# Optimization experiments

Hardware: AMD Instinct MI355X
Metric: run time of the kernel (lower is better)

The kernel has to match this reference:

```python
import jax, jax.numpy as jnp
import numpy as np

B, T, C, H, M = 2, 2048, 1024, 16, 64
EPS = 1e-5


def _ln(x, g, b):
    mu = jnp.mean(x, axis=-1, keepdims=True)
    var = jnp.mean(jnp.square(x - mu), axis=-1, keepdims=True)
    return (x - mu) * jax.lax.rsqrt(var + EPS) * g + b


def setup_inputs() -> dict:
    key = jax.random.key(0)
    ks = jax.random.split(key, 16)
    s = lambda fan_in: 1.0 / np.sqrt(fan_in)
    return {
        'x': jax.random.normal(ks[0], (B, T, C), jnp.float32),
        'ln1_g': jnp.ones((C,), jnp.float32),
        'ln1_b': jnp.zeros((C,), jnp.float32),
        'attn_w': jax.random.normal(ks[1], (C, 3 * C), jnp.float32) * s(C),
        'attn_b': jnp.zeros((3 * C,), jnp.float32),
        'proj_w': jax.random.normal(ks[2], (C, C), jnp.float32) * s(C),
        'proj_b': jnp.zeros((C,), jnp.float32),
        'a1_dw': jax.random.normal(ks[3], (C, M), jnp.float32) * s(C),
        'a1_db': jnp.zeros((M,), jnp.float32),
        'a1_uw': jax.random.normal(ks[4], (M, C), jnp.float32) * s(M),
        'a1_ub': jnp.zeros((C,), jnp.float32),
        'ln2_g': jnp.ones((C,), jnp.float32),
        'ln2_b': jnp.zeros((C,), jnp.float32),
        'fc_w': jax.random.normal(ks[5], (C, 4 * C), jnp.float32) * s(C),
        'fc_b': jnp.zeros((4 * C,), jnp.float32),
        'mlp_pw': jax.random.normal(ks[6], (4 * C, C), jnp.float32) * s(4 * C),
        'mlp_pb': jnp.zeros((C,), jnp.float32),
        'a2_dw': jax.random.normal(ks[7], (C, M), jnp.float32) * s(C),
        'a2_db': jnp.zeros((M,), jnp.float32),
        'a2_uw': jax.random.normal(ks[8], (M, C), jnp.float32) * s(M),
        'a2_ub': jnp.zeros((C,), jnp.float32),
    }


def _attn(x, attn_w, attn_b, proj_w, proj_b):
    b, t, c = x.shape
    hd = c // H
    qkv = x @ attn_w + attn_b                      # [B,T,3C]
    q, k, v = jnp.split(qkv, 3, axis=-1)
    q = q.reshape(b, t, H, hd).transpose(0, 2, 1, 3)  # [B,H,T,hd]
    k = k.reshape(b, t, H, hd).transpose(0, 2, 1, 3)
    v = v.reshape(b, t, H, hd).transpose(0, 2, 1, 3)
    att = jnp.einsum('bhqd,bhkd->bhqk', q, k) * (1.0 / np.sqrt(hd))
    mask = jnp.tril(jnp.ones((t, t), bool))
    att = jnp.where(mask, att, -jnp.inf)
    att = jax.nn.softmax(att, axis=-1)
    y = jnp.einsum('bhqk,bhkd->bhqd', att, v)      # [B,H,T,hd]
    y = y.transpose(0, 2, 1, 3).reshape(b, t, c)
    return y @ proj_w + proj_b


def _adapter(x, dw, db, uw, ub):
    return jax.nn.relu(x @ dw + db) @ uw + ub


def reference(x, ln1_g, ln1_b, attn_w, attn_b, proj_w, proj_b,
              a1_dw, a1_db, a1_uw, a1_ub, ln2_g, ln2_b,
              fc_w, fc_b, mlp_pw, mlp_pb, a2_dw, a2_db, a2_uw, a2_ub):
    x = x + _attn(_ln(x, ln1_g, ln1_b), attn_w, attn_b, proj_w, proj_b)
    x = x + _adapter(x, a1_dw, a1_db, a1_uw, a1_ub)
    h = _ln(x, ln2_g, ln2_b)
    h = jax.nn.gelu(h @ fc_w + fc_b, approximate=True) @ mlp_pw + mlp_pb
    x = x + h
    x = x + _adapter(x, a2_dw, a2_db, a2_uw, a2_ub)
    return x
```

## Files before the change

### kernel.cpp

```cpp
#include <hip/hip_runtime.h>
#include <hip/hip_bf16.h>
#include <cstdint>

#define DEVI __device__ __forceinline__

using bf16x8 = __attribute__((ext_vector_type(8))) short;
using f32x4  = __attribute__((ext_vector_type(4))) float;

DEVI short f2b(float f) {
  __hip_bfloat16 h = __float2bfloat16(f);
  return *reinterpret_cast<short*>(&h);
}
DEVI float b2f(short s) {
  __hip_bfloat16 h = *reinterpret_cast<__hip_bfloat16*>(&s);
  return __bfloat162float(h);
}
DEVI uint32_t pk2(float a, float b) {
  return (uint32_t)(uint16_t)f2b(a) | ((uint32_t)(uint16_t)f2b(b) << 16);
}

DEVI f32x4 mfma16(bf16x8 a, bf16x8 b, f32x4 c) {
  return __builtin_amdgcn_mfma_f32_16x16x32_bf16(a, b, c, 0, 0, 0);
}

DEVI void gload_lds16(const void* g, void* l) {
  __builtin_amdgcn_global_load_lds(
      (const __attribute__((address_space(1))) void*)g,
      (__attribute__((address_space(3))) void*)l, 16, 0, 0);
}

DEVI float gelu_f(float x) {
  float u = 1.5957691216057308f * (x + 0.044715f * x * x * x);
  float e = __expf(u);
  float t = 1.f - 2.f / (e + 1.f);
  return 0.5f * x * (1.f + t);
}

__global__ void k_wt(const float* __restrict__ in, short* __restrict__ out,
                     int R, int Cc) {
  __shared__ float tile[32][33];
  int c0 = blockIdx.x * 32;
  int r0 = blockIdx.y * 32;
  int tx = threadIdx.x, ty = threadIdx.y;
  for (int i = ty; i < 32; i += 8) {
    int r = r0 + i, c = c0 + tx;
    tile[i][tx] = (r < R && c < Cc) ? in[(size_t)r * Cc + c] : 0.f;
  }
  __syncthreads();
  for (int i = ty; i < 32; i += 8) {
    int orow = c0 + i;
    int ocol = r0 + tx;
    if (orow < Cc && ocol < R) out[(size_t)orow * R + ocol] = f2b(tile[tx][i]);
  }
}

__global__ void k_layernorm(const float* __restrict__ x, const float* __restrict__ g,
                            const float* __restrict__ bta, short* __restrict__ out) {
  const int C = 1024;
  int row = blockIdx.x;
  const float* xr = x + (size_t)row * C;
  f32x4 v = *(const f32x4*)(xr + threadIdx.x * 4);
  float s = v[0] + v[1] + v[2] + v[3];
  float s2 = v[0]*v[0] + v[1]*v[1] + v[2]*v[2] + v[3]*v[3];
#pragma unroll
  for (int m = 1; m < 64; m <<= 1) { s += __shfl_xor(s, m); s2 += __shfl_xor(s2, m); }
  __shared__ float red[8];
  int w = threadIdx.x >> 6;
  if ((threadIdx.x & 63) == 0) { red[w] = s; red[4 + w] = s2; }
  __syncthreads();
  s = red[0] + red[1] + red[2] + red[3];
  s2 = red[4] + red[5] + red[6] + red[7];
  float mu = s * (1.f / 1024.f);
  float rstd = rsqrtf(s2 * (1.f / 1024.f) - mu * mu + 1e-5f);
#pragma unroll
  for (int j = 0; j < 4; ++j) {
    int c = threadIdx.x * 4 + j;
    out[(size_t)row * C + c] = f2b((v[j] - mu) * rstd * g[c] + bta[c]);
  }
}

__global__ void k_vtrans(const short* __restrict__ qkv, short* __restrict__ vT) {
  __shared__ short tile[32][72];
  int b = blockIdx.z, h = blockIdx.y;
  int t0 = blockIdx.x * 32;
  int tx = threadIdx.x;
  int ty = threadIdx.y;
  const size_t inbase = ((size_t)(b * 2048 + t0)) * 3072 + 2048 + h * 64;
  for (int i = ty; i < 32; i += 8) {
    tile[i][tx]      = qkv[inbase + (size_t)i * 3072 + tx];
    tile[i][tx + 32] = qkv[inbase + (size_t)i * 3072 + tx + 32];
  }
  __syncthreads();
  const size_t outbase = ((size_t)(b * 16 + h) * 64) * 2048 + t0;
  for (int d = ty; d < 64; d += 8)
    vT[outbase + (size_t)d * 2048 + tx] = tile[tx][d];
}

template <int BM, int BN, int WGM, int WGN, int ACT, bool RESID, bool OUTF, bool OUTB>
__global__ __launch_bounds__(256, 2) void k_gemm(
    const short* __restrict__ A, const short* __restrict__ BT,
    const float* __restrict__ bias, const float* __restrict__ resid,
    float* __restrict__ outf, short* __restrict__ outb,
    int M, int N, int K) {
  static_assert(WGM * WGN == 4, "4 waves");
  constexpr int TM = BM / WGM, TN = BN / WGN;
  constexpr int FM = TM / 16, FN = TN / 16;
  __shared__ short As[BM * 32];
  __shared__ short Bs[BN * 32];
  const int tid = threadIdx.x;
  const int wid = tid >> 6, l = tid & 63, lr = l & 15, lg = l >> 4;
  const int wm = wid / WGN, wn = wid % WGN;
  const int rowA0 = blockIdx.x * BM;
  const int colB0 = blockIdx.y * BN;

  f32x4 acc[FM][FN];
#pragma unroll
  for (int i = 0; i < FM; ++i)
#pragma unroll
    for (int j = 0; j < FN; ++j) acc[i][j] = f32x4{0.f, 0.f, 0.f, 0.f};

  for (int k0 = 0; k0 < K; k0 += 32) {
    __syncthreads();
#pragma unroll
    for (int it = 0; it < (BM * 64) / 4096; ++it) {
      int bo = it * 4096 + tid * 16;
      int row = bo >> 6, col = (bo & 63) >> 1;
      gload_lds16(A + (size_t)(rowA0 + row) * K + k0 + col, (void*)(As + (bo >> 1)));
    }
#pragma unroll
    for (int it = 0; it < (BN * 64) / 4096; ++it) {
      int bo = it * 4096 + tid * 16;
      int row = bo >> 6, col = (bo & 63) >> 1;
      gload_lds16(BT + (size_t)(colB0 + row) * K + k0 + col, (void*)(Bs + (bo >> 1)));
    }
    __syncthreads();
    bf16x8 af[FM], bfr[FN];
#pragma unroll
    for (int i = 0; i < FM; ++i)
      af[i] = *(const bf16x8*)(As + (wm * TM + i * 16 + lr) * 32 + lg * 8);
#pragma unroll
    for (int j = 0; j < FN; ++j)
      bfr[j] = *(const bf16x8*)(Bs + (wn * TN + j * 16 + lr) * 32 + lg * 8);
#pragma unroll
    for (int i = 0; i < FM; ++i)
#pragma unroll
      for (int j = 0; j < FN; ++j)
        acc[i][j] = mfma16(af[i], bfr[j], acc[i][j]);
  }

  const int row0 = rowA0 + wm * TM + lg * 4;
  const int col0 = colB0 + wn * TN + lr;
#pragma unroll
  for (int i = 0; i < FM; ++i) {
#pragma unroll
    for (int j = 0; j < FN; ++j) {
#pragma unroll
      for (int r = 0; r < 4; ++r) {
        int row = row0 + i * 16 + r;
        int col = col0 + j * 16;
        float v = acc[i][j][r] + bias[col];
        if (ACT == 1) v = fmaxf(v, 0.f);
        if (ACT == 2) v = gelu_f(v);
        size_t idx = (size_t)row * N + col;
        if (RESID) v += resid[idx];
        if (OUTF) outf[idx] = v;
        if (OUTB) outb[idx] = f2b(v);
      }
    }
  }
}

__global__ __launch_bounds__(256, 4) void k_attn(
    const short* __restrict__ qkv, const short* __restrict__ vT,
    short* __restrict__ y) {
  constexpr int T = 2048, C3 = 3072;
  const int tid = threadIdx.x;
  const int wid = tid >> 6, l = tid & 63, lr = l & 15, lg = l >> 4;
  const int bh = blockIdx.x, b = bh >> 4, h = bh & 15;
  const int qt = (int)(gridDim.y - 1 - blockIdx.y);
  const int q0 = qt * 64 + wid * 16;

  __shared__ short Plds[4][16][32];

  const float qscale = 0.125f * 1.4426950408889634f;
  const short* qptr = qkv + (size_t)(b * T + q0 + lr) * C3 + h * 64;
  bf16x8 qr0 = *(const bf16x8*)(qptr + lg * 8);
  bf16x8 qr1 = *(const bf16x8*)(qptr + 32 + lg * 8);
  bf16x8 qf0, qf1;
#pragma unroll
  for (int j = 0; j < 8; ++j) {
    qf0[j] = f2b(b2f(qr0[j]) * qscale);
    qf1[j] = f2b(b2f(qr1[j]) * qscale);
  }

  const short* kbase = qkv + (size_t)(b * T) * C3 + 1024 + h * 64;
  const short* vtb = vT + (size_t)bh * 64 * 2048;

  f32x4 o[4];
#pragma unroll
  for (int d = 0; d < 4; ++d) o[d] = f32x4{0.f, 0.f, 0.f, 0.f};
  float m = -1e30f, lsum = 0.f;

  const int kv_full = q0 & ~31;

  auto body = [&](int kv0, bool mask) {
    const short* kp = kbase + (size_t)(kv0 + lr) * C3;
    bf16x8 kf00 = *(const bf16x8*)(kp + lg * 8);
    bf16x8 kf01 = *(const bf16x8*)(kp + 32 + lg * 8);
    const short* kp1 = kp + (size_t)16 * C3;
    bf16x8 kf10 = *(const bf16x8*)(kp1 + lg * 8);
    bf16x8 kf11 = *(const bf16x8*)(kp1 + 32 + lg * 8);
    f32x4 s0 = {0.f, 0.f, 0.f, 0.f}, s1 = {0.f, 0.f, 0.f, 0.f};
    s0 = mfma16(kf00, qf0, s0);
    s0 = mfma16(kf01, qf1, s0);
    s1 = mfma16(kf10, qf0, s1);
    s1 = mfma16(kf11, qf1, s1);
    if (mask) {
      const int q = q0 + lr;
#pragma unroll
      for (int r = 0; r < 4; ++r) {
        if (kv0 + lg * 4 + r > q) s0[r] = -1e30f;
        if (kv0 + 16 + lg * 4 + r > q) s1[r] = -1e30f;
      }
    }
    float mx = fmaxf(fmaxf(fmaxf(s0[0], s0[1]), fmaxf(s0[2], s0[3])),
                     fmaxf(fmaxf(s1[0], s1[1]), fmaxf(s1[2], s1[3])));
    mx = fmaxf(mx, __shfl_xor(mx, 16));
    mx = fmaxf(mx, __shfl_xor(mx, 32));
    if (__any(mx > m + 8.f)) {
      float mn = fmaxf(m, mx);
      float corr = exp2f(m - mn);
      m = mn;
      lsum *= corr;
#pragma unroll
      for (int d = 0; d < 4; ++d)
#pragma unroll
        for (int r = 0; r < 4; ++r) o[d][r] *= corr;
    }
    float p0 = exp2f(s0[0] - m), p1 = exp2f(s0[1] - m);
    float p2 = exp2f(s0[2] - m), p3 = exp2f(s0[3] - m);
    float p4 = exp2f(s1[0] - m), p5 = exp2f(s1[1] - m);
    float p6 = exp2f(s1[2] - m), p7 = exp2f(s1[3] - m);
    lsum += ((p0 + p1) + (p2 + p3)) + ((p4 + p5) + (p6 + p7));
    uint2 w0, w1;
    w0.x = pk2(p0, p1); w0.y = pk2(p2, p3);
    w1.x = pk2(p4, p5); w1.y = pk2(p6, p7);
    *(uint2*)&Plds[wid][lr][lg * 4] = w0;
    *(uint2*)&Plds[wid][lr][16 + lg * 4] = w1;
    bf16x8 pf = *(const bf16x8*)&Plds[wid][lr][lg * 8];
#pragma unroll
    for (int dt = 0; dt < 4; ++dt) {
      bf16x8 vf = *(const bf16x8*)(vtb + (size_t)(dt * 16 + lr) * 2048 + kv0 + lg * 8);
      o[dt] = mfma16(vf, pf, o[dt]);
    }
  };

  for (int kv0 = 0; kv0 < kv_full; kv0 += 32) body(kv0, false);
  body(kv_full, true);

  lsum += __shfl_xor(lsum, 16);
  lsum += __shfl_xor(lsum, 32);
  float inv = 1.f / lsum;

  short* yp = y + (size_t)(b * T + q0 + lr) * 1024 + h * 64;
#pragma unroll
  for (int dt = 0; dt < 4; ++dt) {
    uint2 wv;
    wv.x = pk2(o[dt][0] * inv, o[dt][1] * inv);
    wv.y = pk2(o[dt][2] * inv, o[dt][3] * inv);
    *(uint2*)(yp + dt * 16 + lg * 4) = wv;
  }
}

extern "C" void kernel_launch(void* const* d_in, const int* in_sizes, int n_in,
                              void* d_out, int out_size, void* d_ws, size_t ws_size,
                              hipStream_t stream) {
  (void)in_sizes; (void)n_in; (void)out_size; (void)ws_size;
  const float* x0     = (const float*)d_in[0];
  const float* ln1_g  = (const float*)d_in[1];
  const float* ln1_b  = (const float*)d_in[2];
  const float* attn_w = (const float*)d_in[3];
  const float* attn_b = (const float*)d_in[4];
  const float* proj_w = (const float*)d_in[5];
  const float* proj_b = (const float*)d_in[6];
  const float* a1_dw  = (const float*)d_in[7];
  const float* a1_db  = (const float*)d_in[8];
  const float* a1_uw  = (const float*)d_in[9];
  const float* a1_ub  = (const float*)d_in[10];
  const float* ln2_g  = (const float*)d_in[11];
  const float* ln2_b  = (const float*)d_in[12];
  const float* fc_w   = (const float*)d_in[13];
  const float* fc_b   = (const float*)d_in[14];
  const float* mlp_pw = (const float*)d_in[15];
  const float* mlp_pb = (const float*)d_in[16];
  const float* a2_dw  = (const float*)d_in[17];
  const float* a2_db  = (const float*)d_in[18];
  const float* a2_uw  = (const float*)d_in[19];
  const float* a2_ub  = (const float*)d_in[20];

  char* ws = (char*)d_ws;
  size_t off = 0;
  auto alloc = [&](size_t bytes) {
    char* p = ws + off;
    off = (off + bytes + 255) & ~(size_t)255;
    return p;
  };

  short* attn_wT = (short*)alloc(3072ull * 1024 * 2);
  short* proj_wT = (short*)alloc(1024ull * 1024 * 2);
  short* fc_wT   = (short*)alloc(4096ull * 1024 * 2);
  short* mlp_pwT = (short*)alloc(1024ull * 4096 * 2);
  short* a1_dwT  = (short*)alloc(64ull * 1024 * 2);
  short* a1_uwT  = (short*)alloc(1024ull * 64 * 2);
  short* a2_dwT  = (short*)alloc(64ull * 1024 * 2);
  short* a2_uwT  = (short*)alloc(1024ull * 64 * 2);
  short* lnb     = (short*)alloc(4096ull * 1024 * 2);
  char*  big     = alloc(4096ull * 4096 * 2);
  short* qkvb    = (short*)big;
  short* vTb     = (short*)(big + 4096ull * 3072 * 2);
  short* fcb     = (short*)big;
  short* yb      = (short*)alloc(4096ull * 1024 * 2);
  float* x1f     = (float*)alloc(4096ull * 1024 * 4);
  float* x2f     = (float*)alloc(4096ull * 1024 * 4);
  short* x1b     = (short*)alloc(4096ull * 1024 * 2);
  short* hb      = (short*)alloc(4096ull * 64 * 2);

  dim3 tb(32, 8);
  k_wt<<<dim3(3072 / 32, 1024 / 32), tb, 0, stream>>>(attn_w, attn_wT, 1024, 3072);
  k_wt<<<dim3(1024 / 32, 1024 / 32), tb, 0, stream>>>(proj_w, proj_wT, 1024, 1024);
  k_wt<<<dim3(4096 / 32, 1024 / 32), tb, 0, stream>>>(fc_w, fc_wT, 1024, 4096);
  k_wt<<<dim3(1024 / 32, 4096 / 32), tb, 0, stream>>>(mlp_pw, mlp_pwT, 4096, 1024);
  k_wt<<<dim3(64 / 32, 1024 / 32), tb, 0, stream>>>(a1_dw, a1_dwT, 1024, 64);
  k_wt<<<dim3(1024 / 32, 64 / 32), tb, 0, stream>>>(a1_uw, a1_uwT, 64, 1024);
  k_wt<<<dim3(64 / 32, 1024 / 32), tb, 0, stream>>>(a2_dw, a2_dwT, 1024, 64);
  k_wt<<<dim3(1024 / 32, 64 / 32), tb, 0, stream>>>(a2_uw, a2_uwT, 64, 1024);

  k_layernorm<<<4096, 256, 0, stream>>>(x0, ln1_g, ln1_b, lnb);

  k_gemm<128, 128, 2, 2, 0, false, false, true><<<dim3(32, 24), 256, 0, stream>>>(
      lnb, attn_wT, attn_b, nullptr, nullptr, qkvb, 4096, 3072, 1024);

  k_vtrans<<<dim3(64, 16, 2), tb, 0, stream>>>(qkvb, vTb);

  k_attn<<<dim3(32, 32), 256, 0, stream>>>(qkvb, vTb, yb);

  k_gemm<128, 128, 2, 2, 0, true, true, true><<<dim3(32, 8), 256, 0, stream>>>(
      yb, proj_wT, proj_b, x0, x1f, x1b, 4096, 1024, 1024);

  k_gemm<64, 64, 2, 2, 1, false, false, true><<<dim3(64, 1), 256, 0, stream>>>(
      x1b, a1_dwT, a1_db, nullptr, nullptr, hb, 4096, 64, 1024);

  k_gemm<128, 128, 2, 2, 0, true, true, false><<<dim3(32, 8), 256, 0, stream>>>(
      hb, a1_uwT, a1_ub, x1f, x2f, nullptr, 4096, 1024, 64);

  k_layernorm<<<4096, 256, 0, stream>>>(x2f, ln2_g, ln2_b, lnb);

  k_gemm<128, 128, 2, 2, 2, false, false, true><<<dim3(32, 32), 256, 0, stream>>>(
      lnb, fc_wT, fc_b, nullptr, nullptr, fcb, 4096, 4096, 1024);

  k_gemm<128, 128, 2, 2, 0, true, true, true><<<dim3(32, 8), 256, 0, stream>>>(
      fcb, mlp_pwT, mlp_pb, x2f, x1f, x1b, 4096, 1024, 4096);

  k_gemm<64, 64, 2, 2, 1, false, false, true><<<dim3(64, 1), 256, 0, stream>>>(
      x1b, a2_dwT, a2_db, nullptr, nullptr, hb, 4096, 64, 1024);

  k_gemm<128, 128, 2, 2, 0, true, true, false><<<dim3(32, 8), 256, 0, stream>>>(
      hb, a2_uwT, a2_ub, x1f, (float*)d_out, nullptr, 4096, 1024, 64);
}
```

Measured before the change: 559.6 us.

## Prefetch K tiles double-buffered and pass P via lane shuffles instead of LDS

Restructures the attention inner loop to double-buffer K fragments, loading the next tile's K while the current tile computes, and issues V loads early. The probability fragment is now rearranged into the MFMA B-operand layout with cross-lane shuffles rather than a round trip through shared memory, which removes the LDS buffer. The causal mask is applied on every tile, and launch bounds drop occupancy to 3 blocks so more registers are available. The aim is to hide global load latency and cut LDS traffic, at the cost of extra compares, selects and shuffles per tile and lower occupancy.

```diff
diff --git a/kernel.cpp b/kernel.cpp
--- a/kernel.cpp
+++ b/kernel.cpp
@@ -170,7 +170,7 @@
   }
 }
 
-__global__ __launch_bounds__(256, 4) void k_attn(
+__global__ __launch_bounds__(256, 3) void k_attn(
     const short* __restrict__ qkv, const short* __restrict__ vT,
     short* __restrict__ y) {
   constexpr int T = 2048, C3 = 3072;
@@ -180,8 +180,6 @@
   const int qt = (int)(gridDim.y - 1 - blockIdx.y);
   const int q0 = qt * 64 + wid * 16;
 
-  __shared__ short Plds[4][16][32];
-
   const float qscale = 0.125f * 1.4426950408889634f;
   const short* qptr = qkv + (size_t)(b * T + q0 + lr) * C3 + h * 64;
   bf16x8 qr0 = *(const bf16x8*)(qptr + lg * 8);
@@ -201,28 +199,37 @@
   for (int d = 0; d < 4; ++d) o[d] = f32x4{0.f, 0.f, 0.f, 0.f};
   float m = -1e30f, lsum = 0.f;
 
-  const int kv_full = q0 & ~31;
-
-  auto body = [&](int kv0, bool mask) {
+  const bool lglt2 = (lg < 2);
+  const bool lg0 = (lg == 0), lg1 = (lg == 1), lg2 = (lg == 2), lg3 = (lg == 3);
+  const int q = q0 + lr;
+
+  auto loadK = [&](bf16x8* kf, int kv0) {
     const short* kp = kbase + (size_t)(kv0 + lr) * C3;
-    bf16x8 kf00 = *(const bf16x8*)(kp + lg * 8);
-    bf16x8 kf01 = *(const bf16x8*)(kp + 32 + lg * 8);
-    const short* kp1 = kp + (size_t)16 * C3;
-    bf16x8 kf10 = *(const bf16x8*)(kp1 + lg * 8);
-    bf16x8 kf11 = *(const bf16x8*)(kp1 + 32 + lg * 8);
+    kf[0] = *(const bf16x8*)(kp + lg * 8);
+    kf[1] = *(const bf16x8*)(kp + 32 + lg * 8);
+    kf[2] = *(const bf16x8*)(kp + 16 * C3 + lg * 8);
+    kf[3] = *(const bf16x8*)(kp + 16 * C3 + 32 + lg * 8);
+  };
+
+  auto tile = [&](bf16x8* kf, bf16x8* knext, int kv0, bool pre) {
+    bf16x8 vf0 = *(const bf16x8*)(vtb + (size_t)(0 * 16 + lr) * 2048 + kv0 + lg * 8);
+    bf16x8 vf1 = *(const bf16x8*)(vtb + (size_t)(1 * 16 + lr) * 2048 + kv0 + lg * 8);
+    bf16x8 vf2 = *(const bf16x8*)(vtb + (size_t)(2 * 16 + lr) * 2048 + kv0 + lg * 8);
+    bf16x8 vf3 = *(const bf16x8*)(vtb + (size_t)(3 * 16 + lr) * 2048 + kv0 + lg * 8);
+    if (pre) loadK(knext, kv0 + 32);
+
     f32x4 s0 = {0.f, 0.f, 0.f, 0.f}, s1 = {0.f, 0.f, 0.f, 0.f};
-    s0 = mfma16(kf00, qf0, s0);
-    s0 = mfma16(kf01, qf1, s0);
-    s1 = mfma16(kf10, qf0, s1);
-    s1 = mfma16(kf11, qf1, s1);
-    if (mask) {
-      const int q = q0 + lr;
-#pragma unroll
-      for (int r = 0; r < 4; ++r) {
-        if (kv0 + lg * 4 + r > q) s0[r] = -1e30f;
-        if (kv0 + 16 + lg * 4 + r > q) s1[r] = -1e30f;
-      }
-    }
+    s0 = mfma16(kf[0], qf0, s0);
+    s0 = mfma16(kf[1], qf1, s0);
+    s1 = mfma16(kf[2], qf0, s1);
+    s1 = mfma16(kf[3], qf1, s1);
+
+#pragma unroll
+    for (int r = 0; r < 4; ++r) {
+      if (kv0 + lg * 4 + r > q) s0[r] = -1e30f;
+      if (kv0 + 16 + lg * 4 + r > q) s1[r] = -1e30f;
+    }
+
     float mx = fmaxf(fmaxf(fmaxf(s0[0], s0[1]), fmaxf(s0[2], s0[3])),
                      fmaxf(fmaxf(s1[0], s1[1]), fmaxf(s1[2], s1[3])));
     mx = fmaxf(mx, __shfl_xor(mx, 16));
@@ -242,21 +249,44 @@
     float p4 = exp2f(s1[0] - m), p5 = exp2f(s1[1] - m);
     float p6 = exp2f(s1[2] - m), p7 = exp2f(s1[3] - m);
     lsum += ((p0 + p1) + (p2 + p3)) + ((p4 + p5) + (p6 + p7));
-    uint2 w0, w1;
-    w0.x = pk2(p0, p1); w0.y = pk2(p2, p3);
-    w1.x = pk2(p4, p5); w1.y = pk2(p6, p7);
-    *(uint2*)&Plds[wid][lr][lg * 4] = w0;
-    *(uint2*)&Plds[wid][lr][16 + lg * 4] = w1;
-    bf16x8 pf = *(const bf16x8*)&Plds[wid][lr][lg * 8];
-#pragma unroll
-    for (int dt = 0; dt < 4; ++dt) {
-      bf16x8 vf = *(const bf16x8*)(vtb + (size_t)(dt * 16 + lr) * 2048 + kv0 + lg * 8);
-      o[dt] = mfma16(vf, pf, o[dt]);
-    }
+
+    uint32_t a0 = pk2(p0, p1), a1 = pk2(p2, p3);
+    uint32_t b0 = pk2(p4, p5), b1 = pk2(p6, p7);
+    uint32_t ux = lglt2 ? b0 : a0;
+    uint32_t uy = lglt2 ? b1 : a1;
+    uint32_t rx0 = (uint32_t)__shfl_xor((int)ux, 32);
+    uint32_t rx1 = (uint32_t)__shfl_xor((int)uy, 32);
+    uint32_t vx = lg1 ? a0 : (lg2 ? b0 : rx0);
+    uint32_t vy = lg1 ? a1 : (lg2 ? b1 : rx1);
+    uint32_t rv0 = (uint32_t)__shfl_xor((int)vx, 16);
+    uint32_t rv1 = (uint32_t)__shfl_xor((int)vy, 16);
+    union {
+      bf16x8 v;
+      uint32_t u[4];
+    } P;
+    P.u[0] = lg0 ? a0 : (lg2 ? rx0 : rv0);
+    P.u[1] = lg0 ? a1 : (lg2 ? rx1 : rv1);
+    P.u[2] = lg3 ? b0 : (lg1 ? rx0 : rv0);
+    P.u[3] = lg3 ? b1 : (lg1 ? rx1 : rv1);
+
+    o[0] = mfma16(vf0, P.v, o[0]);
+    o[1] = mfma16(vf1, P.v, o[1]);
+    o[2] = mfma16(vf2, P.v, o[2]);
+    o[3] = mfma16(vf3, P.v, o[3]);
   };
 
-  for (int kv0 = 0; kv0 < kv_full; kv0 += 32) body(kv0, false);
-  body(kv_full, true);
+  bf16x8 KA[4], KB[4];
+  loadK(KA, 0);
+  const int n = (q0 >> 5) + 1;
+  int t = 0, kv0 = 0;
+  while (true) {
+    tile(KA, KB, kv0, t + 1 < n);
+    ++t; kv0 += 32;
+    if (t == n) break;
+    tile(KB, KA, kv0, t + 1 < n);
+    ++t; kv0 += 32;
+    if (t == n) break;
+  }
 
   lsum += __shfl_xor(lsum, 16);
   lsum += __shfl_xor(lsum, 32);
```

New measurement: 551.6 us. Within noise of the previous version (-1.4%).
